# Kernel optimization log

Hardware: AMD Instinct MI355X
Metric: run time of the kernel (lower is better)

Reference implementation:

```python
import jax, jax.numpy as jnp
import numpy as np

N = 100000   # nodes
E = 1600000  # edges
IN = 64      # in_dim
HID = 64     # hid_dim
OUT = 2      # out_dim (sensitive-attribute classes)


def _xavier(key, shape):
    fan_out, fan_in = shape
    lim = np.sqrt(6.0 / (fan_in + fan_out)).astype(np.float32)
    return jax.random.uniform(key, shape, jnp.float32, -lim, lim)


def setup_inputs() -> dict:
    key = jax.random.key(0)
    ks = jax.random.split(key, 10)
    emb_cat = jax.random.normal(ks[0], (E, 2 * HID), jnp.float32)
    features = jax.random.normal(ks[1], (N, IN), jnp.float32)
    edge_index = jax.random.randint(ks[2], (2, E), 0, N)
    labels = jax.random.uniform(ks[3], (N,), jnp.float32)
    # variant_infer: Linear(2*hid -> 1) + Sigmoid
    Wv = _xavier(ks[4], (1, 2 * HID)); bv = jnp.zeros((1,), jnp.float32)
    # GCNConv layer 1 (in_dim -> hid) and layer 2 (hid -> hid)
    W1 = _xavier(ks[5], (HID, IN)); b1 = jnp.zeros((HID,), jnp.float32)
    W2 = _xavier(ks[6], (HID, HID)); b2 = jnp.zeros((HID,), jnp.float32)
    # sens_infer_classifier: Linear(hid+1 -> out) + Softmax
    Wc = _xavier(ks[7], (OUT, HID + 1)); bc = jnp.zeros((OUT,), jnp.float32)
    return {"emb_cat": emb_cat, "features": features, "labels": labels,
            "Wv": Wv, "bv": bv, "W1": W1, "b1": b1, "W2": W2, "b2": b2,
            "Wc": Wc, "bc": bc, "edge_index": edge_index}


def _gcn_layer(x, W, b, src, dst, ew):
    """PyG GCNConv with edge_weight: x@W.T, add self-loops (weight 1),
    symmetric deg^{-1/2} normalization, scatter-sum to target, + bias."""
    x = x @ W.T                                   # [N, out]
    loop = jnp.arange(N)
    s = jnp.concatenate([src, loop])
    d = jnp.concatenate([dst, loop])
    w = jnp.concatenate([ew, jnp.ones((N,), x.dtype)])
    deg = jax.ops.segment_sum(w, d, num_segments=N)  # weighted in-degree
    dis = jnp.where(deg > 0, jax.lax.rsqrt(jnp.where(deg > 0, deg, 1.0)), 0.0)
    norm = dis[s] * w * dis[d]                    # [E+N]
    msg = norm[:, None] * x[s]                    # gather + scale
    return jax.ops.segment_sum(msg, d, num_segments=N) + b


def reference(emb_cat, features, labels, Wv, bv, W1, b1, W2, b2, Wc, bc, edge_index):
    # variant_infer: per-edge weight in (0,1)
    ew = jax.nn.sigmoid(emb_cat @ Wv.T + bv)[:, 0]   # [E]
    src, dst = edge_index[0], edge_index[1]
    # ConstructModel('gcn', layer_num=2): GCNConv -> ReLU -> GCNConv
    h = _gcn_layer(features, W1, b1, src, dst, ew)
    h = jax.nn.relu(h)
    h = _gcn_layer(h, W2, b2, src, dst, ew)
    # sens_infer_classifier on cat([h, labels], dim=1)
    logits = jnp.concatenate([h, labels[:, None]], axis=1) @ Wc.T + bc
    sens = jax.nn.softmax(logits, axis=1)
    return sens, 1.0 - ew
```

## Files before the change

kernel.cpp:

```cpp
#include <hip/hip_runtime.h>
#include <hip/hip_bf16.h>
#include <hip/hip_fp16.h>
#include <math.h>

typedef unsigned long long u64;

#define SHIFT 10
#define BSZ   1024
#define MAXBK 128
#define EPB   4096

__global__ __launch_bounds__(256) void k_edge_ew(
    const float* __restrict__ emb, const float* __restrict__ Wv, const float* __restrict__ bv,
    float* __restrict__ out_ew, int E)
{
    int grp = blockIdx.x * 8 + (threadIdx.x >> 5);
    int base = grp * 4;
    if (base >= E) return;
    int l = threadIdx.x & 31;
    const float4* embp = (const float4*)emb;
    const float4 w = ((const float4*)Wv)[l];
    float dot[4];
#pragma unroll
    for (int q = 0; q < 4; ++q) {
        const float4 v = embp[(size_t)(base + q) * 32 + l];
        dot[q] = v.x * w.x + v.y * w.y + v.z * w.z + v.w * w.w;
    }
#pragma unroll
    for (int m = 16; m >= 1; m >>= 1) {
#pragma unroll
        for (int q = 0; q < 4; ++q) dot[q] += __shfl_xor(dot[q], m);
    }
    if (l == 0) {
        float bv0 = bv[0];
        float s[4];
#pragma unroll
        for (int q = 0; q < 4; ++q) s[q] = 1.0f / (1.0f + expf(-(dot[q] + bv0)));
        float4 o = {1.0f - s[0], 1.0f - s[1], 1.0f - s[2], 1.0f - s[3]};
        ((float4*)out_ew)[grp] = o;
    }
}

__global__ __launch_bounds__(256) void k_hist(const int* __restrict__ dst, int* __restrict__ ghist,
                                              int* __restrict__ done, int E, int nbk, int nblk)
{
    __shared__ int h[MAXBK];
    int t = threadIdx.x, b = blockIdx.x;
    if (b == 0 && t == 0) done[0] = 0;
    if (t < nbk) h[t] = 0;
    __syncthreads();
    int base = b * EPB, end = min(base + EPB, E);
    for (int i = base + t; i < end; i += 256) atomicAdd(&h[dst[i] >> SHIFT], 1);
    __syncthreads();
    if (t < nbk) ghist[t * nblk + b] = h[t];
}

__global__ __launch_bounds__(512) void k_scan_col(int* __restrict__ ghist, int* __restrict__ btot,
                                                  int* __restrict__ bstart, int* __restrict__ done,
                                                  int nblk, int nbk)
{
    __shared__ int sA[512], sB[512];
    __shared__ int isLast;
    int k = blockIdx.x, t = threadIdx.x;
    int v = (t < nblk) ? ghist[k * nblk + t] : 0;
    sA[t] = v; __syncthreads();
    int* cur = sA; int* nxt = sB;
    for (int off = 1; off < 512; off <<= 1) {
        int x = cur[t];
        if (t >= off) x += cur[t - off];
        nxt[t] = x; __syncthreads();
        int* tmp = cur; cur = nxt; nxt = tmp;
    }
    if (t < nblk) ghist[k * nblk + t] = cur[t] - v;
    if (t == 511) btot[k] = cur[511];
    __threadfence();
    if (t == 0) isLast = (atomicAdd(done, 1) == gridDim.x - 1);
    __syncthreads();
    if (!isLast) return;
    __threadfence();
    int bv2 = (t < nbk) ? btot[t] : 0;
    sA[t] = bv2; __syncthreads();
    cur = sA; nxt = sB;
    for (int off = 1; off < 512; off <<= 1) {
        int x = cur[t];
        if (t >= off) x += cur[t - off];
        nxt[t] = x; __syncthreads();
        int* tmp = cur; cur = nxt; nxt = tmp;
    }
    if (t < nbk) bstart[t] = cur[t] - bv2;
    if (t == nbk - 1) bstart[nbk] = cur[t];
}

__global__ __launch_bounds__(256) void k_scatter(
    const int* __restrict__ src, const int* __restrict__ dst, const float* __restrict__ out_ew,
    const int* __restrict__ ghist, const int* __restrict__ bstart,
    u64* __restrict__ tmp, int E, int nbk, int nblk)
{
    __shared__ int lofs[MAXBK + 1];
    __shared__ int lcur[MAXBK];
    __shared__ int gdst[MAXBK];
    __shared__ int pA[128], pB[128];
    __shared__ u64 recs[EPB];
    int t = threadIdx.x, b = blockIdx.x;
    if (t < nbk) lcur[t] = 0;
    __syncthreads();
    int base = b * EPB, end = min(base + EPB, E);
    for (int i = base + t; i < end; i += 256) atomicAdd(&lcur[dst[i] >> SHIFT], 1);
    __syncthreads();
    int v0 = 0;
    if (t < 128) { v0 = (t < nbk) ? lcur[t] : 0; pA[t] = v0; }
    __syncthreads();
    int* cu = pA; int* nx = pB;
    for (int off = 1; off < 128; off <<= 1) {
        int x = 0;
        if (t < 128) { x = cu[t]; if (t >= off) x += cu[t - off]; }
        __syncthreads();
        if (t < 128) nx[t] = x;
        __syncthreads();
        int* tp = cu; cu = nx; nx = tp;
    }
    if (t < nbk) lofs[t] = cu[t] - v0;
    if (t == nbk - 1) lofs[nbk] = cu[t];
    __syncthreads();
    if (t < nbk) {
        lcur[t] = lofs[t];
        gdst[t] = bstart[t] + ghist[t * nblk + b];
    }
    __syncthreads();
    for (int i = base + t; i < end; i += 256) {
        int d = dst[i];
        int k = d >> SHIFT;
        int p = atomicAdd(&lcur[k], 1);
        float w = 1.0f - out_ew[i];
        recs[p] = ((u64)__float_as_uint(w) << 32) | ((u64)(unsigned)(d & (BSZ - 1)) << 17)
                | (u64)(unsigned)src[i];
    }
    __syncthreads();
    int total = end - base;
    for (int j = t; j < total; j += 256) {
        int lo = 0, hi = nbk;
        while (hi - lo > 1) {
            int mid = (lo + hi) >> 1;
            if (lofs[mid] <= j) lo = mid; else hi = mid;
        }
        tmp[gdst[lo] + (j - lofs[lo])] = recs[j];
    }
}

__global__ __launch_bounds__(512) void k_build(
    const u64* __restrict__ tmp, const int* __restrict__ bstart,
    u64* __restrict__ edat, int* __restrict__ rowptr, int* __restrict__ cnt,
    float* __restrict__ deg, int N)
{
    __shared__ int   lcnt[BSZ];
    __shared__ int   lcur[BSZ];
    __shared__ float ldeg[BSZ];
    __shared__ int   sA[512], sB[512];
    int k = blockIdx.x, t = threadIdx.x;
    int nodeBase = k * BSZ;
    int r0 = bstart[k], r1 = bstart[k + 1];
    for (int i = t; i < BSZ; i += 512) { lcnt[i] = 0; ldeg[i] = 1.0f; }
    __syncthreads();
    for (int i = r0 + t; i < r1; i += 512) {
        u64 rec = tmp[i];
        int dl = (int)((rec >> 17) & (BSZ - 1));
        atomicAdd(&lcnt[dl], 1);
        atomicAdd(&ldeg[dl], __uint_as_float((unsigned)(rec >> 32)));
    }
    __syncthreads();
    int a = lcnt[2 * t], bb = lcnt[2 * t + 1];
    sA[t] = a + bb; __syncthreads();
    int* cur = sA; int* nxt = sB;
    for (int off = 1; off < 512; off <<= 1) {
        int x = cur[t];
        if (t >= off) x += cur[t - off];
        nxt[t] = x; __syncthreads();
        int* tp = cur; cur = nxt; nxt = tp;
    }
    int excl = cur[t] - (a + bb);
    lcur[2 * t] = excl;
    lcur[2 * t + 1] = excl + a;
    __syncthreads();
    for (int i = t; i < BSZ; i += 512) {
        int node = nodeBase + i;
        if (node < N) {
            rowptr[node] = r0 + lcur[i];
            cnt[node]    = lcnt[i];
            deg[node]    = ldeg[i];
        }
    }
    __syncthreads();
    for (int i = r0 + t; i < r1; i += 512) {
        u64 rec = tmp[i];
        int dl = (int)((rec >> 17) & (BSZ - 1));
        int p = atomicAdd(&lcur[dl], 1);
        edat[r0 + p] = ((rec >> 32) << 32) | (rec & 0x1FFFFull);
    }
}

__global__ __launch_bounds__(256) void k_gemm64h(
    const float* __restrict__ X, const float* __restrict__ W, const float* __restrict__ deg,
    __half* __restrict__ Y, int n)
{
    __shared__ float w[64][64];
    for (int i = threadIdx.x; i < 64 * 64; i += 256) w[i >> 6][i & 63] = W[i];
    __syncthreads();
    int node = blockIdx.x * 256 + threadIdx.x;
    if (node >= n) return;
    float r[64];
    const float4* xr = (const float4*)(X + (size_t)node * 64);
#pragma unroll
    for (int q = 0; q < 16; ++q) {
        float4 v = xr[q];
        r[4 * q] = v.x; r[4 * q + 1] = v.y; r[4 * q + 2] = v.z; r[4 * q + 3] = v.w;
    }
    float ds = rsqrtf(deg[node]);
    uint2* yr = (uint2*)(Y + (size_t)node * 64);
    for (int j = 0; j < 64; j += 4) {
        float a0 = 0.f, a1 = 0.f, a2 = 0.f, a3 = 0.f;
#pragma unroll
        for (int kk = 0; kk < 64; ++kk) {
            a0 += r[kk] * w[j][kk];
            a1 += r[kk] * w[j + 1][kk];
            a2 += r[kk] * w[j + 2][kk];
            a3 += r[kk] * w[j + 3][kk];
        }
        __half2 h01 = __floats2half2_rn(ds * a0, ds * a1);
        __half2 h23 = __floats2half2_rn(ds * a2, ds * a3);
        uint2 pk;
        pk.x = *(unsigned*)&h01;
        pk.y = *(unsigned*)&h23;
        yr[j >> 2] = pk;
    }
}

__device__ __forceinline__ float2 agg_node2(const __half2* __restrict__ A2, const u64* __restrict__ ed,
                                            int c, int lane)
{
    int g = lane >> 5;
    int l = lane & 31;
    float2 acc = {0.f, 0.f};
    int jb = 0;
    for (; jb + 16 <= c; jb += 16) {
        u64 myrec = ed[jb + (lane & 15)];
        u64 rec[8];
#pragma unroll
        for (int q = 0; q < 8; ++q) rec[q] = __shfl(myrec, 2 * q + g);
        unsigned raw[8];
#pragma unroll
        for (int q = 0; q < 8; ++q) {
            int s = (int)(unsigned)(rec[q] & 0xffffffffu);
            raw[q] = *(const unsigned*)&A2[(size_t)s * 32 + l];
        }
#pragma unroll
        for (int q = 0; q < 8; ++q) {
            float w = __uint_as_float((unsigned)(rec[q] >> 32));
            float2 v = __half22float2(*(__half2*)&raw[q]);
            acc.x += w * v.x;
            acc.y += w * v.y;
        }
    }
    if (jb < c) {
        int cm1 = c - 1;
        u64 myrec = ed[min(jb + (lane & 15), cm1)];
        u64 rec[8];
#pragma unroll
        for (int q = 0; q < 8; ++q) rec[q] = __shfl(myrec, 2 * q + g);
        unsigned raw[8];
#pragma unroll
        for (int q = 0; q < 8; ++q) {
            int s = (int)(unsigned)(rec[q] & 0xffffffffu);
            raw[q] = *(const unsigned*)&A2[(size_t)s * 32 + l];
        }
#pragma unroll
        for (int q = 0; q < 8; ++q) {
            int idx = jb + 2 * q + g;
            float w = (idx < c) ? __uint_as_float((unsigned)(rec[q] >> 32)) : 0.f;
            float2 v = __half22float2(*(__half2*)&raw[q]);
            acc.x += w * v.x;
            acc.y += w * v.y;
        }
    }
    acc.x += __shfl_xor(acc.x, 32);
    acc.y += __shfl_xor(acc.y, 32);
    return acc;
}

__global__ __launch_bounds__(256) void k_agg1(
    const __half* __restrict__ A, const int* __restrict__ rowptr, const int* __restrict__ cnt,
    const u64* __restrict__ edat, const float* __restrict__ deg,
    const float* __restrict__ b1, float* __restrict__ H, int N)
{
    int node = blockIdx.x * 4 + (threadIdx.x >> 6);
    if (node >= N) return;
    int lane = threadIdx.x & 63;
    int l = lane & 31;
    const __half2* A2 = (const __half2*)A;
    float2 acc = agg_node2(A2, edat + rowptr[node], cnt[node], lane);
    float dsd = rsqrtf(deg[node]);
    float2 self = __half22float2(A2[(size_t)node * 32 + l]);
    float2 bb = ((const float2*)b1)[l];
    if (lane < 32) {
        float2 h;
        h.x = fmaxf(dsd * (acc.x + self.x) + bb.x, 0.f);
        h.y = fmaxf(dsd * (acc.y + self.y) + bb.y, 0.f);
        ((float2*)(H + (size_t)node * 64))[l] = h;
    }
}

__global__ __launch_bounds__(256) void k_agg2_final(
    const __half* __restrict__ A, const int* __restrict__ rowptr, const int* __restrict__ cnt,
    const u64* __restrict__ edat, const float* __restrict__ deg,
    const float* __restrict__ b2, const float* __restrict__ labels,
    const float* __restrict__ Wc, const float* __restrict__ bc,
    float* __restrict__ out, int N)
{
    int node = blockIdx.x * 4 + (threadIdx.x >> 6);
    if (node >= N) return;
    int lane = threadIdx.x & 63;
    int l = lane & 31;
    const __half2* A2 = (const __half2*)A;
    float2 acc = agg_node2(A2, edat + rowptr[node], cnt[node], lane);
    float dsd = rsqrtf(deg[node]);
    float2 self = __half22float2(A2[(size_t)node * 32 + l]);
    float2 bb = ((const float2*)b2)[l];
    float hx = dsd * (acc.x + self.x) + bb.x;
    float hy = dsd * (acc.y + self.y) + bb.y;
    float2 wc0 = ((const float2*)Wc)[l];
    float w1x = Wc[65 + 2 * l], w1y = Wc[65 + 2 * l + 1];
    float p0 = hx * wc0.x + hy * wc0.y;
    float p1 = hx * w1x + hy * w1y;
    if (lane >= 32) { p0 = 0.f; p1 = 0.f; }
#pragma unroll
    for (int mm = 1; mm < 64; mm <<= 1) {
        p0 += __shfl_xor(p0, mm);
        p1 += __shfl_xor(p1, mm);
    }
    if (lane == 0) {
        float lab = labels[node];
        float l0 = p0 + lab * Wc[64] + bc[0];
        float l1 = p1 + lab * Wc[65 + 64] + bc[1];
        float mx = fmaxf(l0, l1);
        float e0 = expf(l0 - mx), e1 = expf(l1 - mx);
        float inv = 1.0f / (e0 + e1);
        out[2 * (size_t)node]     = e0 * inv;
        out[2 * (size_t)node + 1] = e1 * inv;
    }
}

extern "C" void kernel_launch(void* const* d_in, const int* in_sizes, int n_in,
                              void* d_out, int out_size, void* d_ws, size_t ws_size,
                              hipStream_t stream)
{
    const float* emb      = (const float*)d_in[0];
    const float* features = (const float*)d_in[1];
    const float* labels   = (const float*)d_in[2];
    const float* Wv       = (const float*)d_in[3];
    const float* bv       = (const float*)d_in[4];
    const float* W1       = (const float*)d_in[5];
    const float* b1       = (const float*)d_in[6];
    const float* W2       = (const float*)d_in[7];
    const float* b2       = (const float*)d_in[8];
    const float* Wc       = (const float*)d_in[9];
    const float* bc       = (const float*)d_in[10];
    const int*   eidx     = (const int*)d_in[11];

    const int E = in_sizes[11] / 2;
    const int N = in_sizes[1] / 64;
    const int* src = eidx;
    const int* dst = eidx + E;

    float* out      = (float*)d_out;
    float* out_sens = out;
    float* out_ew   = out + 2 * (size_t)N;

    const int nbk  = (N + BSZ - 1) >> SHIFT;
    const int nblk = (E + EPB - 1) / EPB;

    float*  deg    = (float*)d_ws;
    __half* Ah     = (__half*)(deg + N);
    float*  H      = (float*)(Ah + (size_t)N * 64);
    int*    cnt    = (int*)(H + (size_t)N * 64);
    int*    rowptr = cnt + N;
    int*    ghist  = rowptr + N;
    int*    btot   = ghist + (size_t)nbk * nblk;
    int*    bstart = btot + nbk;
    int*    done   = bstart + nbk + 1;
    size_t  ofs4   = (size_t)((done + 1) - (int*)d_ws);
    ofs4 = (ofs4 + 1) & ~(size_t)1;
    u64*    tmp    = (u64*)((int*)d_ws + ofs4);
    u64*    edat   = tmp + E;

    k_edge_ew<<<(E / 4 + 7) / 8, 256, 0, stream>>>(emb, Wv, bv, out_ew, E);

    k_hist<<<nblk, 256, 0, stream>>>(dst, ghist, done, E, nbk, nblk);
    k_scan_col<<<nbk, 512, 0, stream>>>(ghist, btot, bstart, done, nblk, nbk);
    k_scatter<<<nblk, 256, 0, stream>>>(src, dst, out_ew, ghist, bstart, tmp, E, nbk, nblk);
    k_build<<<nbk, 512, 0, stream>>>(tmp, bstart, edat, rowptr, cnt, deg, N);

    k_gemm64h<<<(N + 255) / 256, 256, 0, stream>>>(features, W1, deg, Ah, N);
    k_agg1<<<(N + 3) / 4, 256, 0, stream>>>(Ah, rowptr, cnt, edat, deg, b1, H, N);

    k_gemm64h<<<(N + 255) / 256, 256, 0, stream>>>(H, W2, deg, Ah, N);
    k_agg2_final<<<(N + 3) / 4, 256, 0, stream>>>(Ah, rowptr, cnt, edat, deg, b2,
                                                  labels, Wc, bc, out_sens, N);
}
```

Before: 427.3 us.

## Fuse edge-weight, histogram and first GEMM into one launch; fuse agg1 with GEMM2

Merges the edge-weight, histogram and layer-1 GEMM kernels into one launch that splits work by block range, so the independent stages run together. The deg^-1/2 scaling of the layer-1 features moves into k_build, which rescales the half-precision rows in place. The layer-1 aggregation now also applies W2 and writes half-precision layer-2 input directly, which removes the fp32 H buffer round trip and one GEMM launch. The cost is extra shared memory in the aggregation kernel, a block-wide sync, and an additional read-modify-write pass over Ah1 inside k_build.

```diff
diff --git a/kernel.cpp b/kernel.cpp
--- a/kernel.cpp
+++ b/kernel.cpp
@@ -10,49 +10,91 @@
 #define MAXBK 128
 #define EPB   4096
 
-__global__ __launch_bounds__(256) void k_edge_ew(
+__global__ __launch_bounds__(256) void k_mega1(
     const float* __restrict__ emb, const float* __restrict__ Wv, const float* __restrict__ bv,
-    float* __restrict__ out_ew, int E)
-{
-    int grp = blockIdx.x * 8 + (threadIdx.x >> 5);
-    int base = grp * 4;
-    if (base >= E) return;
-    int l = threadIdx.x & 31;
-    const float4* embp = (const float4*)emb;
-    const float4 w = ((const float4*)Wv)[l];
-    float dot[4];
-#pragma unroll
-    for (int q = 0; q < 4; ++q) {
-        const float4 v = embp[(size_t)(base + q) * 32 + l];
-        dot[q] = v.x * w.x + v.y * w.y + v.z * w.z + v.w * w.w;
-    }
-#pragma unroll
-    for (int m = 16; m >= 1; m >>= 1) {
-#pragma unroll
-        for (int q = 0; q < 4; ++q) dot[q] += __shfl_xor(dot[q], m);
-    }
-    if (l == 0) {
-        float bv0 = bv[0];
-        float s[4];
-#pragma unroll
-        for (int q = 0; q < 4; ++q) s[q] = 1.0f / (1.0f + expf(-(dot[q] + bv0)));
-        float4 o = {1.0f - s[0], 1.0f - s[1], 1.0f - s[2], 1.0f - s[3]};
-        ((float4*)out_ew)[grp] = o;
-    }
-}
-
-__global__ __launch_bounds__(256) void k_hist(const int* __restrict__ dst, int* __restrict__ ghist,
-                                              int* __restrict__ done, int E, int nbk, int nblk)
-{
-    __shared__ int h[MAXBK];
-    int t = threadIdx.x, b = blockIdx.x;
-    if (b == 0 && t == 0) done[0] = 0;
-    if (t < nbk) h[t] = 0;
-    __syncthreads();
-    int base = b * EPB, end = min(base + EPB, E);
-    for (int i = base + t; i < end; i += 256) atomicAdd(&h[dst[i] >> SHIFT], 1);
-    __syncthreads();
-    if (t < nbk) ghist[t * nblk + b] = h[t];
+    float* __restrict__ out_ew, int E,
+    const int* __restrict__ dst, int* __restrict__ ghist, int* __restrict__ done,
+    int nbk, int nblk,
+    const float* __restrict__ X, const float* __restrict__ W1, __half* __restrict__ Yh, int N,
+    int bEW, int bH)
+{
+    __shared__ float smemf[4096];
+    int b = blockIdx.x, t = threadIdx.x;
+
+    if (b < bEW) {
+        int grp = b * 8 + (t >> 5);
+        size_t base = (size_t)grp * 8;
+        int l = t & 31;
+        const float4* embp = (const float4*)emb;
+        const float4 w = ((const float4*)Wv)[l];
+        float dot[8];
+#pragma unroll
+        for (int q = 0; q < 8; ++q) {
+            const float4 v = embp[(base + q) * 32 + l];
+            dot[q] = v.x * w.x + v.y * w.y + v.z * w.z + v.w * w.w;
+        }
+#pragma unroll
+        for (int m = 16; m >= 1; m >>= 1) {
+#pragma unroll
+            for (int q = 0; q < 8; ++q) dot[q] += __shfl_xor(dot[q], m);
+        }
+        if (l == 0) {
+            float bv0 = bv[0];
+            float o[8];
+#pragma unroll
+            for (int q = 0; q < 8; ++q) o[q] = 1.0f - 1.0f / (1.0f + expf(-(dot[q] + bv0)));
+            float4 o0 = {o[0], o[1], o[2], o[3]};
+            float4 o1 = {o[4], o[5], o[6], o[7]};
+            ((float4*)out_ew)[2 * grp]     = o0;
+            ((float4*)out_ew)[2 * grp + 1] = o1;
+        }
+        return;
+    }
+    b -= bEW;
+    if (b < bH) {
+        int* h = (int*)smemf;
+        if (b == 0 && t == 0) done[0] = 0;
+        if (t < nbk) h[t] = 0;
+        __syncthreads();
+        int base = b * EPB, end = min(base + EPB, E);
+        for (int i = base + t; i < end; i += 256) atomicAdd(&h[dst[i] >> SHIFT], 1);
+        __syncthreads();
+        if (t < nbk) ghist[t * nblk + b] = h[t];
+        return;
+    }
+    b -= bH;
+    {
+        float (*w)[64] = (float(*)[64])smemf;
+        for (int i = t; i < 4096; i += 256) w[i >> 6][i & 63] = W1[i];
+        __syncthreads();
+        int node = b * 256 + t;
+        if (node >= N) return;
+        float r[64];
+        const float4* xr = (const float4*)(X + (size_t)node * 64);
+#pragma unroll
+        for (int q = 0; q < 16; ++q) {
+            float4 v = xr[q];
+            r[4 * q] = v.x; r[4 * q + 1] = v.y; r[4 * q + 2] = v.z; r[4 * q + 3] = v.w;
+        }
+        uint2* yr = (uint2*)(Yh + (size_t)node * 64);
+        for (int j = 0; j < 64; j += 4) {
+            float a0 = 0.f, a1 = 0.f, a2 = 0.f, a3 = 0.f;
+#pragma unroll
+            for (int kk = 0; kk < 64; ++kk) {
+                a0 += r[kk] * w[j][kk];
+                a1 += r[kk] * w[j + 1][kk];
+                a2 += r[kk] * w[j + 2][kk];
+                a3 += r[kk] * w[j + 3][kk];
+            }
+            __half2 h01 = __floats2half2_rn(a0, a1);
+            __half2 h23 = __floats2half2_rn(a2, a3);
+            uint2 pk;
+            pk.x = *(unsigned*)&h01;
+            pk.y = *(unsigned*)&h23;
+            yr[j >> 2] = pk;
+        }
+        return;
+    }
 }
 
 __global__ __launch_bounds__(512) void k_scan_col(int* __restrict__ ghist, int* __restrict__ btot,
@@ -150,7 +192,7 @@
 __global__ __launch_bounds__(512) void k_build(
     const u64* __restrict__ tmp, const int* __restrict__ bstart,
     u64* __restrict__ edat, int* __restrict__ rowptr, int* __restrict__ cnt,
-    float* __restrict__ deg, int N)
+    float* __restrict__ deg, __half* __restrict__ Ah, int N)
 {
     __shared__ int   lcnt[BSZ];
     __shared__ int   lcur[BSZ];
@@ -196,41 +238,15 @@
         int p = atomicAdd(&lcur[dl], 1);
         edat[r0 + p] = ((rec >> 32) << 32) | (rec & 0x1FFFFull);
     }
-}
-
-__global__ __launch_bounds__(256) void k_gemm64h(
-    const float* __restrict__ X, const float* __restrict__ W, const float* __restrict__ deg,
-    __half* __restrict__ Y, int n)
-{
-    __shared__ float w[64][64];
-    for (int i = threadIdx.x; i < 64 * 64; i += 256) w[i >> 6][i & 63] = W[i];
-    __syncthreads();
-    int node = blockIdx.x * 256 + threadIdx.x;
-    if (node >= n) return;
-    float r[64];
-    const float4* xr = (const float4*)(X + (size_t)node * 64);
-#pragma unroll
-    for (int q = 0; q < 16; ++q) {
-        float4 v = xr[q];
-        r[4 * q] = v.x; r[4 * q + 1] = v.y; r[4 * q + 2] = v.z; r[4 * q + 3] = v.w;
-    }
-    float ds = rsqrtf(deg[node]);
-    uint2* yr = (uint2*)(Y + (size_t)node * 64);
-    for (int j = 0; j < 64; j += 4) {
-        float a0 = 0.f, a1 = 0.f, a2 = 0.f, a3 = 0.f;
-#pragma unroll
-        for (int kk = 0; kk < 64; ++kk) {
-            a0 += r[kk] * w[j][kk];
-            a1 += r[kk] * w[j + 1][kk];
-            a2 += r[kk] * w[j + 2][kk];
-            a3 += r[kk] * w[j + 3][kk];
-        }
-        __half2 h01 = __floats2half2_rn(ds * a0, ds * a1);
-        __half2 h23 = __floats2half2_rn(ds * a2, ds * a3);
-        uint2 pk;
-        pk.x = *(unsigned*)&h01;
-        pk.y = *(unsigned*)&h23;
-        yr[j >> 2] = pk;
+    __half2* A2 = (__half2*)Ah;
+    for (int idx = t; idx < BSZ * 32; idx += 512) {
+        int ni = idx >> 5;
+        int node = nodeBase + ni;
+        if (node < N) {
+            float f = rsqrtf(ldeg[ni]);
+            float2 v = __half22float2(A2[(size_t)node * 32 + (idx & 31)]);
+            A2[(size_t)node * 32 + (idx & 31)] = __floats2half2_rn(f * v.x, f * v.y);
+        }
     }
 }
 
@@ -286,26 +302,37 @@
     return acc;
 }
 
-__global__ __launch_bounds__(256) void k_agg1(
+__global__ __launch_bounds__(256) void k_agg1g2(
     const __half* __restrict__ A, const int* __restrict__ rowptr, const int* __restrict__ cnt,
     const u64* __restrict__ edat, const float* __restrict__ deg,
-    const float* __restrict__ b1, float* __restrict__ H, int N)
-{
-    int node = blockIdx.x * 4 + (threadIdx.x >> 6);
-    if (node >= N) return;
-    int lane = threadIdx.x & 63;
-    int l = lane & 31;
+    const float* __restrict__ b1, const float* __restrict__ W2,
+    __half* __restrict__ Y2, int N)
+{
+    __shared__ float w2[64][65];
+    __shared__ float hbuf[4][64];
+    int t = threadIdx.x;
+    for (int i = t; i < 4096; i += 256) w2[i >> 6][i & 63] = W2[i];
+    int wid = t >> 6, lane = t & 63, l = lane & 31;
+    int node = blockIdx.x * 4 + wid;
+    if (node >= N) node = N - 1;
     const __half2* A2 = (const __half2*)A;
     float2 acc = agg_node2(A2, edat + rowptr[node], cnt[node], lane);
-    float dsd = rsqrtf(deg[node]);
+    float ds = rsqrtf(deg[node]);
     float2 self = __half22float2(A2[(size_t)node * 32 + l]);
     float2 bb = ((const float2*)b1)[l];
-    if (lane < 32) {
-        float2 h;
-        h.x = fmaxf(dsd * (acc.x + self.x) + bb.x, 0.f);
-        h.y = fmaxf(dsd * (acc.y + self.y) + bb.y, 0.f);
-        ((float2*)(H + (size_t)node * 64))[l] = h;
-    }
+    float2 h;
+    h.x = fmaxf(ds * (acc.x + self.x) + bb.x, 0.f);
+    h.y = fmaxf(ds * (acc.y + self.y) + bb.y, 0.f);
+    if (lane < 32) ((float2*)hbuf[wid])[l] = h;
+    __syncthreads();
+    float a = 0.f;
+#pragma unroll 8
+    for (int k = 0; k < 64; ++k) a += hbuf[wid][k] * w2[lane][k];
+    float y = ds * a;
+    float ye = __shfl(y, 2 * l);
+    float yo = __shfl(y, 2 * l + 1);
+    if (lane < 32)
+        ((__half2*)Y2)[(size_t)node * 32 + l] = __floats2half2_rn(ye, yo);
 }
 
 __global__ __launch_bounds__(256) void k_agg2_final(
@@ -378,9 +405,9 @@
     const int nblk = (E + EPB - 1) / EPB;
 
     float*  deg    = (float*)d_ws;
-    __half* Ah     = (__half*)(deg + N);
-    float*  H      = (float*)(Ah + (size_t)N * 64);
-    int*    cnt    = (int*)(H + (size_t)N * 64);
+    __half* Ah1    = (__half*)(deg + N);
+    __half* Ah2    = (__half*)((int*)(deg + N) + (size_t)N * 32);
+    int*    cnt    = (int*)((int*)Ah2 + (size_t)N * 32);
     int*    rowptr = cnt + N;
     int*    ghist  = rowptr + N;
     int*    btot   = ghist + (size_t)nbk * nblk;
@@ -391,17 +418,18 @@
     u64*    tmp    = (u64*)((int*)d_ws + ofs4);
     u64*    edat   = tmp + E;
 
-    k_edge_ew<<<(E / 4 + 7) / 8, 256, 0, stream>>>(emb, Wv, bv, out_ew, E);
-
-    k_hist<<<nblk, 256, 0, stream>>>(dst, ghist, done, E, nbk, nblk);
+    const int bEW = E / 64;
+    const int bGM = (N + 255) / 256;
+
+    k_mega1<<<bEW + nblk + bGM, 256, 0, stream>>>(emb, Wv, bv, out_ew, E,
+                                                  dst, ghist, done, nbk, nblk,
+                                                  features, W1, Ah1, N, bEW, nblk);
     k_scan_col<<<nbk, 512, 0, stream>>>(ghist, btot, bstart, done, nblk, nbk);
     k_scatter<<<nblk, 256, 0, stream>>>(src, dst, out_ew, ghist, bstart, tmp, E, nbk, nblk);
-    k_build<<<nbk, 512, 0, stream>>>(tmp, bstart, edat, rowptr, cnt, deg, N);
-
-    k_gemm64h<<<(N + 255) / 256, 256, 0, stream>>>(features, W1, deg, Ah, N);
-    k_agg1<<<(N + 3) / 4, 256, 0, stream>>>(Ah, rowptr, cnt, edat, deg, b1, H, N);
-
-    k_gemm64h<<<(N + 255) / 256, 256, 0, stream>>>(H, W2, deg, Ah, N);
-    k_agg2_final<<<(N + 3) / 4, 256, 0, stream>>>(Ah, rowptr, cnt, edat, deg, b2,
+    k_build<<<nbk, 512, 0, stream>>>(tmp, bstart, edat, rowptr, cnt, deg, Ah1, N);
+
+    k_agg1g2<<<(N + 3) / 4, 256, 0, stream>>>(Ah1, rowptr, cnt, edat, deg, b1, W2, Ah2, N);
+
+    k_agg2_final<<<(N + 3) / 4, 256, 0, stream>>>(Ah2, rowptr, cnt, edat, deg, b2,
                                                   labels, Wc, bc, out_sens, N);
 }
```

New measurement: 444.9 us. 4.1% more time.
